# Kernel optimization log

Hardware: AMD Instinct MI355X
Metric: run time of the kernel (lower is better)

## Reference

```python
import jax, jax.numpy as jnp
import numpy as np

ACT_BIT = 8
WEIGHT_BIT = 8
BIAS_BIT = 32
EPS = 1e-8


def _sym_scale(sat_max, bit):
    # symmetric_linear_quantization_params: scale = clamp(sat, 1e-8) / (2^(b-1)-1)
    n = 2 ** (bit - 1) - 1
    return jnp.maximum(sat_max, EPS) / n


def _sym_quant(x, scale, bit):
    # SymmetricQuantFunction: round(x/scale) clamped to [-2^(b-1), 2^(b-1)-1]
    n = 2 ** (bit - 1) - 1
    return jnp.clip(jnp.round(x / scale), -n - 1, n)


def setup_inputs() -> dict:
    key = jax.random.key(0)
    kx, kw, kb = jax.random.split(key, 3)
    B, S, D_IN, D_OUT = 4, 2048, 4096, 4096
    x = jax.random.normal(kx, (B, S, D_IN), dtype=jnp.float32)
    W = jax.random.normal(kw, (D_OUT, D_IN), dtype=jnp.float32) * 0.02
    b = jax.random.normal(kb, (D_OUT,), dtype=jnp.float32) * 0.02
    return {"x": x, "W": W, "b": b}


def reference(x, W, b):
    # --- QuantAct (per-tensor symmetric int8, min/max from x itself) ---
    x_min, x_max = x.min(), x.max()
    act_scale = _sym_scale(jnp.maximum(jnp.abs(x_min), jnp.abs(x_max)), ACT_BIT)
    x_int = _sym_quant(x, act_scale, ACT_BIT)  # [B,S,Din], int values in fp32

    # --- QuantLinearBase (per-tensor symmetric int8 weight, int32 bias) ---
    w_sat = jnp.maximum(jnp.abs(W.min()), jnp.abs(W.max()))
    w_scale = _sym_scale(w_sat, WEIGHT_BIT)
    w_int = _sym_quant(W, w_scale, WEIGHT_BIT)  # [Dout,Din]

    bias_scale = act_scale * w_scale
    n32 = 2 ** (BIAS_BIT - 1) - 1
    b_int = jnp.clip(jnp.round(b / bias_scale), -n32 - 1, n32)  # [Dout]

    # integer GEMM + bias, then rescale by act_scale * w_scale
    out_int = jnp.einsum("bsi,oi->bso", x_int, w_int) + b_int
    return out_int * bias_scale
```

## Files before the change

kernel.cpp:

```cpp
#include <hip/hip_runtime.h>
#include <cstdint>
#include <cstddef>


typedef int v4i __attribute__((ext_vector_type(4)));

__device__ __forceinline__ void async_copy16(const void* g, void* s) {
  __builtin_amdgcn_global_load_lds(
      (const __attribute__((address_space(1))) void*)g,
      (__attribute__((address_space(3))) void*)s, 16, 0, 0);
}

__device__ __forceinline__ float block_max(float m) {
  __shared__ float smax[4];
#pragma unroll
  for (int off = 32; off > 0; off >>= 1)
    m = fmaxf(m, __shfl_down(m, off, 64));
  if ((threadIdx.x & 63) == 0) smax[threadIdx.x >> 6] = m;
  __syncthreads();
  return fmaxf(fmaxf(smax[0], smax[1]), fmaxf(smax[2], smax[3]));
}

#define NBX 1024
#define NBW 512

__global__ __launch_bounds__(256) void absmax_partial_kernel(
    const float4* __restrict__ x, int xn4, const float4* __restrict__ w,
    int wn4, float* __restrict__ px, float* __restrict__ pw) {
  const float4* src;
  float* dst;
  int n4, bid, nb;
  if (blockIdx.x < NBX) {
    src = x; n4 = xn4; dst = px; bid = blockIdx.x; nb = NBX;
  } else {
    src = w; n4 = wn4; dst = pw; bid = blockIdx.x - NBX; nb = NBW;
  }
  float m = 0.0f;
  for (int i = bid * 256 + threadIdx.x; i < n4; i += nb * 256) {
    float4 v = src[i];
    m = fmaxf(m, fmaxf(fmaxf(fabsf(v.x), fabsf(v.y)),
                       fmaxf(fabsf(v.z), fabsf(v.w))));
  }
  m = block_max(m);
  if (threadIdx.x == 0) dst[bid] = m;
}

__global__ __launch_bounds__(256) void absmax_final_kernel(
    const float* __restrict__ px, const float* __restrict__ pw,
    float* __restrict__ sat) {
  const float* src = (blockIdx.x == 0) ? px : pw;
  const int n = (blockIdx.x == 0) ? NBX : NBW;
  float m = 0.0f;
  for (int i = threadIdx.x; i < n; i += 256) m = fmaxf(m, src[i]);
  m = block_max(m);
  if (threadIdx.x == 0) sat[blockIdx.x] = m;
}

__global__ __launch_bounds__(256) void quant_fused_kernel(
    const float4* __restrict__ x, int xn4, const float4* __restrict__ w,
    int wn4, const float* __restrict__ sat, int* __restrict__ xq,
    int* __restrict__ wq) {
  int i = blockIdx.x * 256 + threadIdx.x;
  float4 v;
  float scale;
  int* q;
  int qi;
  if (i < xn4) {
    v = x[i];
    scale = fmaxf(sat[0], 1e-8f) / 127.0f;
    q = xq; qi = i;
  } else {
    int j = i - xn4;
    if (j >= wn4) return;
    v = w[j];
    scale = fmaxf(sat[1], 1e-8f) / 127.0f;
    q = wq; qi = j;
  }
  int a = (int)fminf(fmaxf(rintf(v.x / scale), -128.0f), 127.0f);
  int b = (int)fminf(fmaxf(rintf(v.y / scale), -128.0f), 127.0f);
  int c = (int)fminf(fmaxf(rintf(v.z / scale), -128.0f), 127.0f);
  int d = (int)fminf(fmaxf(rintf(v.w / scale), -128.0f), 127.0f);
  q[qi] = (a & 255) | ((b & 255) << 8) | ((c & 255) << 16) | ((d & 255) << 24);
}

__global__ __launch_bounds__(256) void i8_gemm_kernel(
    const signed char* __restrict__ Aq, const signed char* __restrict__ Bq,
    const float* __restrict__ bias, const float* __restrict__ sat,
    float* __restrict__ out, int M, int N, int K) {
  __shared__ signed char Als[128 * 64];
  __shared__ signed char Bls[128 * 64];

  const int tid = threadIdx.x;
  const int lane = tid & 63;
  const int wave = tid >> 6;
  const int wm = (wave & 1) * 64;
  const int wn = (wave >> 1) * 64;
  const int M0 = blockIdx.y * 128;
  const int N0 = blockIdx.x * 128;

  const int srow = tid >> 2;
  const int sb = tid & 3;
  const int cg = sb ^ ((srow >> 1) & 3);
  const signed char* Ag = Aq + (size_t)(M0 + srow) * K + cg * 16;
  const signed char* Bg = Bq + (size_t)(N0 + srow) * K + cg * 16;
  signed char* AlsP = &Als[srow * 64 + sb * 16];
  signed char* BlsP = &Bls[srow * 64 + sb * 16];

  v4i acc[4][4] = {};

  const int r15 = lane & 15;
  const int swz = (r15 >> 1) & 3;
  const int kb = ((lane >> 4) ^ swz) * 16;

  for (int kt = 0; kt < K; kt += 64) {
    __syncthreads();
    async_copy16(Ag + kt, AlsP);
    async_copy16(Ag + kt + (size_t)64 * K, AlsP + 64 * 64);
    async_copy16(Bg + kt, BlsP);
    async_copy16(Bg + kt + (size_t)64 * K, BlsP + 64 * 64);
    __syncthreads();

    v4i af[4], bf[4];
#pragma unroll
    for (int t = 0; t < 4; ++t) {
      af[t] = *(const v4i*)&Als[(wm + t * 16 + r15) * 64 + kb];
      bf[t] = *(const v4i*)&Bls[(wn + t * 16 + r15) * 64 + kb];
    }
#pragma unroll
    for (int tm = 0; tm < 4; ++tm)
#pragma unroll
      for (int tn = 0; tn < 4; ++tn)
        acc[tm][tn] = __builtin_amdgcn_mfma_i32_16x16x64_i8(
            af[tm], bf[tn], acc[tm][tn], 0, 0, 0);
  }

  const float act_s = fmaxf(sat[0], 1e-8f) / 127.0f;
  const float w_s = fmaxf(sat[1], 1e-8f) / 127.0f;
  const float bscale = act_s * w_s;

#pragma unroll
  for (int tn = 0; tn < 4; ++tn) {
    const int col = N0 + wn + tn * 16 + r15;
    const float fb = rintf(bias[col] / bscale);
#pragma unroll
    for (int tm = 0; tm < 4; ++tm) {
      const int row0 = M0 + wm + tm * 16 + (lane >> 4) * 4;
#pragma unroll
      for (int r = 0; r < 4; ++r) {
        out[(size_t)(row0 + r) * N + col] =
            ((float)acc[tm][tn][r] + fb) * bscale;
      }
    }
  }
}

extern "C" void kernel_launch(void* const* d_in, const int* in_sizes, int n_in,
                              void* d_out, int out_size, void* d_ws,
                              size_t ws_size, hipStream_t stream) {
  const float* x = (const float*)d_in[0];
  const float* W = (const float*)d_in[1];
  const float* b = (const float*)d_in[2];
  float* out = (float*)d_out;

  const int Dout = in_sizes[2];
  const int K = in_sizes[1] / Dout;
  const int M = in_sizes[0] / K;
  const int N = Dout;

  float* sat = (float*)d_ws;
  float* px = sat + 16;
  float* pw = px + NBX;
  signed char* xq = (signed char*)d_ws + 8192;
  signed char* wq = xq + (size_t)M * K;

  const int xn4 = in_sizes[0] / 4;
  const int wn4 = in_sizes[1] / 4;

  absmax_partial_kernel<<<NBX + NBW, 256, 0, stream>>>(
      (const float4*)x, xn4, (const float4*)W, wn4, px, pw);
  absmax_final_kernel<<<2, 256, 0, stream>>>(px, pw, sat);
  quant_fused_kernel<<<(xn4 + wn4 + 255) / 256, 256, 0, stream>>>(
      (const float4*)x, xn4, (const float4*)W, wn4, sat, (int*)xq, (int*)wq);

  dim3 grid(N / 128, M / 128);
  i8_gemm_kernel<<<grid, 256, 0, stream>>>(xq, wq, b, sat, out, M, N, K);
}
```

Baseline: 478.4 us.

## Widen GEMM K-tile, remap block order, stage epilogue via LDS, unroll prep kernels

The GEMM K-tile doubles to 128 with an 8-way XOR swizzle, so there are half as many barrier pairs per K. A 1D grid is remapped into 8 M-groups for better L2 locality. The epilogue now stages results through LDS so the output is written as coalesced float4 stores. The absmax and quant kernels switch to grid-stride loops with 4-way unrolled loads and more absmax blocks. LDS use doubles to 32 KB, which may lower occupancy, and there is still no double buffering.

```diff
diff --git a/kernel.cpp b/kernel.cpp
--- a/kernel.cpp
+++ b/kernel.cpp
@@ -9,6 +9,10 @@
   __builtin_amdgcn_global_load_lds(
       (const __attribute__((address_space(1))) void*)g,
       (__attribute__((address_space(3))) void*)s, 16, 0, 0);
+}
+
+__device__ __forceinline__ float max4(float4 v) {
+  return fmaxf(fmaxf(fabsf(v.x), fabsf(v.y)), fmaxf(fabsf(v.z), fabsf(v.w)));
 }
 
 __device__ __forceinline__ float block_max(float m) {
@@ -21,8 +25,8 @@
   return fmaxf(fmaxf(smax[0], smax[1]), fmaxf(smax[2], smax[3]));
 }
 
-#define NBX 1024
-#define NBW 512
+#define NBX 2048
+#define NBW 1024
 
 __global__ __launch_bounds__(256) void absmax_partial_kernel(
     const float4* __restrict__ x, int xn4, const float4* __restrict__ w,
@@ -35,12 +39,14 @@
   } else {
     src = w; n4 = wn4; dst = pw; bid = blockIdx.x - NBX; nb = NBW;
   }
+  const int s = nb * 256;
   float m = 0.0f;
-  for (int i = bid * 256 + threadIdx.x; i < n4; i += nb * 256) {
-    float4 v = src[i];
-    m = fmaxf(m, fmaxf(fmaxf(fabsf(v.x), fabsf(v.y)),
-                       fmaxf(fabsf(v.z), fabsf(v.w))));
-  }
+  int i = bid * 256 + threadIdx.x;
+  for (; i + 3 * s < n4; i += 4 * s) {
+    float4 a = src[i], b = src[i + s], c = src[i + 2 * s], d = src[i + 3 * s];
+    m = fmaxf(m, fmaxf(fmaxf(max4(a), max4(b)), fmaxf(max4(c), max4(d))));
+  }
+  for (; i < n4; i += s) m = fmaxf(m, max4(src[i]));
   m = block_max(m);
   if (threadIdx.x == 0) dst[bid] = m;
 }
@@ -56,100 +62,138 @@
   if (threadIdx.x == 0) sat[blockIdx.x] = m;
 }
 
+__device__ __forceinline__ int quant4(float4 v, float scale) {
+  int a = (int)fminf(fmaxf(rintf(v.x / scale), -128.0f), 127.0f);
+  int b = (int)fminf(fmaxf(rintf(v.y / scale), -128.0f), 127.0f);
+  int c = (int)fminf(fmaxf(rintf(v.z / scale), -128.0f), 127.0f);
+  int d = (int)fminf(fmaxf(rintf(v.w / scale), -128.0f), 127.0f);
+  return (a & 255) | ((b & 255) << 8) | ((c & 255) << 16) | ((d & 255) << 24);
+}
+
+#define QBX 4096
+#define QBW 2048
+
 __global__ __launch_bounds__(256) void quant_fused_kernel(
     const float4* __restrict__ x, int xn4, const float4* __restrict__ w,
     int wn4, const float* __restrict__ sat, int* __restrict__ xq,
     int* __restrict__ wq) {
-  int i = blockIdx.x * 256 + threadIdx.x;
-  float4 v;
+  const float4* src;
+  int* q;
+  int n4, bid, nb;
   float scale;
-  int* q;
-  int qi;
-  if (i < xn4) {
-    v = x[i];
+  if (blockIdx.x < QBX) {
+    src = x; q = xq; n4 = xn4; bid = blockIdx.x; nb = QBX;
     scale = fmaxf(sat[0], 1e-8f) / 127.0f;
-    q = xq; qi = i;
   } else {
-    int j = i - xn4;
-    if (j >= wn4) return;
-    v = w[j];
+    src = w; q = wq; n4 = wn4; bid = blockIdx.x - QBX; nb = QBW;
     scale = fmaxf(sat[1], 1e-8f) / 127.0f;
-    q = wq; qi = j;
-  }
-  int a = (int)fminf(fmaxf(rintf(v.x / scale), -128.0f), 127.0f);
-  int b = (int)fminf(fmaxf(rintf(v.y / scale), -128.0f), 127.0f);
-  int c = (int)fminf(fmaxf(rintf(v.z / scale), -128.0f), 127.0f);
-  int d = (int)fminf(fmaxf(rintf(v.w / scale), -128.0f), 127.0f);
-  q[qi] = (a & 255) | ((b & 255) << 8) | ((c & 255) << 16) | ((d & 255) << 24);
+  }
+  const int s = nb * 256;
+  int i = bid * 256 + threadIdx.x;
+  for (; i + 3 * s < n4; i += 4 * s) {
+    float4 a = src[i], b = src[i + s], c = src[i + 2 * s], d = src[i + 3 * s];
+    q[i] = quant4(a, scale);
+    q[i + s] = quant4(b, scale);
+    q[i + 2 * s] = quant4(c, scale);
+    q[i + 3 * s] = quant4(d, scale);
+  }
+  for (; i < n4; i += s) q[i] = quant4(src[i], scale);
 }
 
 __global__ __launch_bounds__(256) void i8_gemm_kernel(
     const signed char* __restrict__ Aq, const signed char* __restrict__ Bq,
     const float* __restrict__ bias, const float* __restrict__ sat,
     float* __restrict__ out, int M, int N, int K) {
-  __shared__ signed char Als[128 * 64];
-  __shared__ signed char Bls[128 * 64];
+  __shared__ __align__(16) signed char smem[2 * 128 * 128];
+  signed char* Als = smem;
+  signed char* Bls = smem + 128 * 128;
 
   const int tid = threadIdx.x;
   const int lane = tid & 63;
   const int wave = tid >> 6;
   const int wm = (wave & 1) * 64;
   const int wn = (wave >> 1) * 64;
-  const int M0 = blockIdx.y * 128;
-  const int N0 = blockIdx.x * 128;
-
-  const int srow = tid >> 2;
-  const int sb = tid & 3;
-  const int cg = sb ^ ((srow >> 1) & 3);
+
+  const int ntn = N >> 7, ntm = M >> 7;
+  int bm, bn;
+  if ((ntm & 7) == 0) {
+    const int g = blockIdx.x & 7;
+    const int j = blockIdx.x >> 3;
+    bm = g * (ntm >> 3) + j / ntn;
+    bn = j % ntn;
+  } else {
+    bm = blockIdx.x / ntn;
+    bn = blockIdx.x % ntn;
+  }
+  const int M0 = bm * 128;
+  const int N0 = bn * 128;
+
+  const int srow = tid >> 3;
+  const int sc = tid & 7;
+  const int cg = sc ^ (srow & 7);
   const signed char* Ag = Aq + (size_t)(M0 + srow) * K + cg * 16;
   const signed char* Bg = Bq + (size_t)(N0 + srow) * K + cg * 16;
-  signed char* AlsP = &Als[srow * 64 + sb * 16];
-  signed char* BlsP = &Bls[srow * 64 + sb * 16];
+  signed char* AlsP = &Als[tid * 16];
+  signed char* BlsP = &Bls[tid * 16];
 
   v4i acc[4][4] = {};
 
   const int r15 = lane & 15;
-  const int swz = (r15 >> 1) & 3;
-  const int kb = ((lane >> 4) ^ swz) * 16;
-
-  for (int kt = 0; kt < K; kt += 64) {
+  const int qd = lane >> 4;
+
+  for (int kt = 0; kt < K; kt += 128) {
     __syncthreads();
-    async_copy16(Ag + kt, AlsP);
-    async_copy16(Ag + kt + (size_t)64 * K, AlsP + 64 * 64);
-    async_copy16(Bg + kt, BlsP);
-    async_copy16(Bg + kt + (size_t)64 * K, BlsP + 64 * 64);
+#pragma unroll
+    for (int p = 0; p < 4; ++p) {
+      async_copy16(Ag + kt + (size_t)(32 * p) * K, AlsP + 4096 * p);
+      async_copy16(Bg + kt + (size_t)(32 * p) * K, BlsP + 4096 * p);
+    }
     __syncthreads();
 
-    v4i af[4], bf[4];
-#pragma unroll
-    for (int t = 0; t < 4; ++t) {
-      af[t] = *(const v4i*)&Als[(wm + t * 16 + r15) * 64 + kb];
-      bf[t] = *(const v4i*)&Bls[(wn + t * 16 + r15) * 64 + kb];
+#pragma unroll
+    for (int h = 0; h < 2; ++h) {
+      v4i af[4], bf[4];
+      const int slot = ((qd + 4 * h) ^ (r15 & 7)) * 16;
+#pragma unroll
+      for (int t = 0; t < 4; ++t) {
+        af[t] = *(const v4i*)&Als[(wm + t * 16 + r15) * 128 + slot];
+        bf[t] = *(const v4i*)&Bls[(wn + t * 16 + r15) * 128 + slot];
+      }
+#pragma unroll
+      for (int tm = 0; tm < 4; ++tm)
+#pragma unroll
+        for (int tn = 0; tn < 4; ++tn)
+          acc[tm][tn] = __builtin_amdgcn_mfma_i32_16x16x64_i8(
+              af[tm], bf[tn], acc[tm][tn], 0, 0, 0);
     }
-#pragma unroll
-    for (int tm = 0; tm < 4; ++tm)
-#pragma unroll
-      for (int tn = 0; tn < 4; ++tn)
-        acc[tm][tn] = __builtin_amdgcn_mfma_i32_16x16x64_i8(
-            af[tm], bf[tn], acc[tm][tn], 0, 0, 0);
   }
 
   const float act_s = fmaxf(sat[0], 1e-8f) / 127.0f;
   const float w_s = fmaxf(sat[1], 1e-8f) / 127.0f;
   const float bscale = act_s * w_s;
 
-#pragma unroll
-  for (int tn = 0; tn < 4; ++tn) {
-    const int col = N0 + wn + tn * 16 + r15;
-    const float fb = rintf(bias[col] / bscale);
-#pragma unroll
-    for (int tm = 0; tm < 4; ++tm) {
-      const int row0 = M0 + wm + tm * 16 + (lane >> 4) * 4;
-#pragma unroll
-      for (int r = 0; r < 4; ++r) {
-        out[(size_t)(row0 + r) * N + col] =
-            ((float)acc[tm][tn][r] + fb) * bscale;
-      }
+  float fb[4];
+#pragma unroll
+  for (int tn = 0; tn < 4; ++tn)
+    fb[tn] = rintf(bias[N0 + wn + tn * 16 + r15] / bscale);
+
+  __syncthreads();
+  float* T = (float*)smem + wave * (16 * 68);
+#pragma unroll
+  for (int tm = 0; tm < 4; ++tm) {
+#pragma unroll
+    for (int tn = 0; tn < 4; ++tn)
+#pragma unroll
+      for (int r = 0; r < 4; ++r)
+        T[(qd * 4 + r) * 68 + tn * 16 + r15] =
+            ((float)acc[tm][tn][r] + fb[tn]) * bscale;
+#pragma unroll
+    for (int p = 0; p < 4; ++p) {
+      const int lr = (p & 1) * 8 + (lane >> 3);
+      const int f4 = (p >> 1) * 8 + (lane & 7);
+      float4 v = *(const float4*)&T[lr * 68 + f4 * 4];
+      *(float4*)&out[(size_t)(M0 + wm + tm * 16 + lr) * N + N0 + wn + f4 * 4] =
+          v;
     }
   }
 }
@@ -170,7 +214,7 @@
   float* sat = (float*)d_ws;
   float* px = sat + 16;
   float* pw = px + NBX;
-  signed char* xq = (signed char*)d_ws + 8192;
+  signed char* xq = (signed char*)d_ws + 16384;
   signed char* wq = xq + (size_t)M * K;
 
   const int xn4 = in_sizes[0] / 4;
@@ -179,9 +223,9 @@
   absmax_partial_kernel<<<NBX + NBW, 256, 0, stream>>>(
       (const float4*)x, xn4, (const float4*)W, wn4, px, pw);
   absmax_final_kernel<<<2, 256, 0, stream>>>(px, pw, sat);
-  quant_fused_kernel<<<(xn4 + wn4 + 255) / 256, 256, 0, stream>>>(
+  quant_fused_kernel<<<QBX + QBW, 256, 0, stream>>>(
       (const float4*)x, xn4, (const float4*)W, wn4, sat, (int*)xq, (int*)wq);
 
-  dim3 grid(N / 128, M / 128);
-  i8_gemm_kernel<<<grid, 256, 0, stream>>>(xq, wq, b, sat, out, M, N, K);
-}
+  i8_gemm_kernel<<<(M / 128) * (N / 128), 256, 0, stream>>>(xq, wq, b, sat,
+                                                            out, M, N, K);
+}
```

Measured after the change: 499.9 us. 1.05x slower.
